# Optimization experiments

Measured on AMD Instinct MI355X. Metric: run time of the kernel, lower is better.

Reference implementation:

```python
import jax, jax.numpy as jnp
import numpy as np

N_NODES = 50000
N_EDGES = 800000
D_IN = 128
D_OUT = 128


def setup_inputs() -> dict:
    key = jax.random.key(0)
    k1, k2, k3, k4, k5 = jax.random.split(key, 5)
    # xavier-uniform-like scale for the two linear layers (gain for relu ~ sqrt(2))
    bound = float(np.sqrt(2.0) * np.sqrt(6.0 / (D_IN + D_OUT)))
    return {
        "feat": jax.random.normal(k1, (N_NODES, D_IN), dtype=jnp.float32),
        "w_neigh": jax.random.uniform(k2, (D_OUT, D_IN), minval=-bound, maxval=bound, dtype=jnp.float32),
        "w_self": jax.random.uniform(k3, (D_OUT, D_IN), minval=-bound, maxval=bound, dtype=jnp.float32),
        "b_self": jnp.zeros((D_OUT,), dtype=jnp.float32),
        "rows": jax.random.randint(k4, (N_EDGES,), 0, N_NODES, dtype=jnp.int32),  # src node per edge
        "cols": jax.random.randint(k5, (N_EDGES,), 0, N_NODES, dtype=jnp.int32),  # dst node per edge
    }


def reference(feat, w_neigh, w_self, b_self, rows, cols):
    n = feat.shape[0]
    # srcdata = fc_neigh(feat): [N, D_OUT]
    srcdata = feat @ w_neigh.T
    # deg[j] = A.sum(0)[j] = in-degree of destination j (column sums)
    deg = jax.ops.segment_sum(jnp.ones_like(cols, dtype=feat.dtype), cols, num_segments=n)
    # dstdata = (A @ diag(deg)^-1).T @ srcdata  ==  mean over incoming src neighbors
    agg = jax.ops.segment_sum(srcdata[rows], cols, num_segments=n)  # [N, D_OUT]
    dstdata = agg / jnp.where(deg > 0, deg, 1.0)[:, None]
    # rst = fc_self(h_self) + dstdata
    return feat @ w_self.T + b_self + dstdata
```

## Files before the change

kernel.cpp:

```cpp
#include <hip/hip_runtime.h>
#include <hip/hip_bf16.h>

#define D 128
#define CAP 64
#define TILE 16

typedef __attribute__((ext_vector_type(8))) short bf16x8;
typedef __attribute__((ext_vector_type(4))) float floatx4;
typedef __attribute__((ext_vector_type(2))) float floatx2;

__device__ __forceinline__ unsigned short f2bf(float f) {
    unsigned int u = __float_as_uint(f);
    return (unsigned short)((u + 0x7fffu + ((u >> 16) & 1u)) >> 16);
}

__global__ __launch_bounds__(256) void zero_kernel(int* __restrict__ p, int n) {
    int i = blockIdx.x * 256 + threadIdx.x;
    if (i < n) p[i] = 0;
}

__global__ __launch_bounds__(256) void prep_fill_kernel(
    const float* __restrict__ feat,
    const float* __restrict__ w_self,
    const float* __restrict__ w_neigh,
    const int* __restrict__ rows,
    const int* __restrict__ cols,
    unsigned int* __restrict__ feat_q,
    unsigned short* __restrict__ ws_h,
    unsigned short* __restrict__ wn_h,
    int* __restrict__ cursor,
    unsigned short* __restrict__ slots,
    int n_nodes, int n_edges)
{
    const int b = blockIdx.x;
    const int tid = threadIdx.x;
    const int role = b % 3;

    if (role < 2) {
        int pb = (b / 3) * 2 + role;
        int i  = pb * 256 + tid;
        if (i < n_nodes * 32) {
            float4 v = *(const float4*)&feat[(long long)4 * i];
            int q = __builtin_amdgcn_cvt_pk_fp8_f32(v.x, v.y, 0, false);
            q = __builtin_amdgcn_cvt_pk_fp8_f32(v.z, v.w, q, true);
            feat_q[i] = (unsigned int)q;
        }
    } else {
        int fb = b / 3;
        int e  = fb * 256 + tid;
        if (e < n_edges) {
            int c = cols[e];
            int p = atomicAdd(&cursor[c], 1);
            if (p < CAP) slots[c * CAP + p] = (unsigned short)rows[e];
        }
        if (fb < 32) {
            int i = fb * 256 + tid;
            int j = i & 4095;
            const float* src = (i < 4096) ? w_self : w_neigh;
            unsigned short* dst = (i < 4096) ? ws_h : wn_h;
            float4 v = *(const float4*)&src[4 * j];
            ushort4 o;
            o.x = f2bf(v.x); o.y = f2bf(v.y); o.z = f2bf(v.z); o.w = f2bf(v.w);
            *(ushort4*)&dst[4 * j] = o;
        }
    }
}

__global__ __launch_bounds__(256, 6) void agg_gemm_kernel(
    const float* __restrict__ feat,
    const unsigned int* __restrict__ feat_q,
    const int* __restrict__ cursor,
    const unsigned short* __restrict__ slots,
    const unsigned short* __restrict__ ws_h,
    const unsigned short* __restrict__ wn_h,
    const float* __restrict__ b_self,
    float* __restrict__ out,
    int n_nodes)
{
    __shared__ unsigned short s_agg[TILE][136];
    __shared__ int s_deg[TILE];

    const int tid  = threadIdx.x;
    const int row0 = blockIdx.x * TILE;

    if (tid < TILE) {
        int node = row0 + tid;
        int d = 0;
        if (node < n_nodes) {
            d = cursor[node];
            if (d > CAP) d = CAP;
        }
        s_deg[tid] = d;
    }
    __syncthreads();

    {
        const int nl  = tid >> 4;
        const int t16 = tid & 15;
        const int sub = t16 & 1;
        const int ln  = t16 >> 1;
        const int deg = s_deg[nl];

        float acc[16];
        #pragma unroll
        for (int i = 0; i < 16; ++i) acc[i] = 0.f;

        const unsigned short* slotp = slots + (long long)(row0 + nl) * CAP;

        for (int k0 = 0; k0 < deg; k0 += 16) {
            uint4 s0 = *(const uint4*)(slotp + k0);
            uint4 s1 = *(const uint4*)(slotp + k0 + 8);
            unsigned int sv[8] = {s0.x, s0.y, s0.z, s0.w, s1.x, s1.y, s1.z, s1.w};
            int cnt = deg - k0; if (cnt > 16) cnt = 16;

            uint4 g[8];
            #pragma unroll
            for (int jj = 0; jj < 8; ++jj) {
                int j = jj * 2 + sub;
                if (j < cnt) {
                    int r = (int)((sv[j >> 1] >> ((j & 1) * 16)) & 0xffffu);
                    g[jj] = *(const uint4*)(feat_q + (long long)r * 32 + ln * 4);
                }
            }
            #pragma unroll
            for (int jj = 0; jj < 8; ++jj) {
                int j = jj * 2 + sub;
                if (j < cnt) {
                    unsigned int wv[4] = {g[jj].x, g[jj].y, g[jj].z, g[jj].w};
                    #pragma unroll
                    for (int c = 0; c < 4; ++c) {
                        floatx2 lo = __builtin_amdgcn_cvt_pk_f32_fp8((int)wv[c], false);
                        floatx2 hi = __builtin_amdgcn_cvt_pk_f32_fp8((int)wv[c], true);
                        acc[c * 4 + 0] += lo.x;
                        acc[c * 4 + 1] += lo.y;
                        acc[c * 4 + 2] += hi.x;
                        acc[c * 4 + 3] += hi.y;
                    }
                }
            }
        }

        #pragma unroll
        for (int i = 0; i < 16; ++i) acc[i] += __shfl_xor(acc[i], 1);

        if (sub == 0) {
            float inv = (deg > 0) ? 1.0f / (float)deg : 0.0f;
            #pragma unroll
            for (int c = 0; c < 4; ++c) {
                ushort4 o;
                o.x = f2bf(acc[c * 4 + 0] * inv);
                o.y = f2bf(acc[c * 4 + 1] * inv);
                o.z = f2bf(acc[c * 4 + 2] * inv);
                o.w = f2bf(acc[c * 4 + 3] * inv);
                *(ushort4*)&s_agg[nl][ln * 16 + c * 4] = o;
            }
        }
    }

    const int wave  = tid >> 6;
    const int lane  = tid & 63;
    const int m     = lane & 15;
    const int quad  = lane >> 4;
    const int kq    = quad * 8;
    const int cbase = wave * 32;

    floatx4 gacc[2];
    gacc[0] = (floatx4){0.f, 0.f, 0.f, 0.f};
    gacc[1] = (floatx4){0.f, 0.f, 0.f, 0.f};

    int rA = row0 + m;
    if (rA > n_nodes - 1) rA = n_nodes - 1;

    #pragma unroll
    for (int kt = 0; kt < 4; ++kt) {
        const int k = kt * 32 + kq;
        float4 f0 = *(const float4*)&feat[(long long)rA * D + k];
        float4 f1 = *(const float4*)&feat[(long long)rA * D + k + 4];
        bf16x8 a;
        a[0] = (short)f2bf(f0.x); a[1] = (short)f2bf(f0.y);
        a[2] = (short)f2bf(f0.z); a[3] = (short)f2bf(f0.w);
        a[4] = (short)f2bf(f1.x); a[5] = (short)f2bf(f1.y);
        a[6] = (short)f2bf(f1.z); a[7] = (short)f2bf(f1.w);
        #pragma unroll
        for (int nt = 0; nt < 2; ++nt) {
            bf16x8 b = *(const bf16x8*)&ws_h[(cbase + nt * 16 + m) * D + k];
            gacc[nt] = __builtin_amdgcn_mfma_f32_16x16x32_bf16(a, b, gacc[nt], 0, 0, 0);
        }
    }

    __syncthreads();

    #pragma unroll
    for (int kt = 0; kt < 4; ++kt) {
        const int k = kt * 32 + kq;
        bf16x8 a = *(const bf16x8*)&s_agg[m][k];
        #pragma unroll
        for (int nt = 0; nt < 2; ++nt) {
            bf16x8 b = *(const bf16x8*)&wn_h[(cbase + nt * 16 + m) * D + k];
            gacc[nt] = __builtin_amdgcn_mfma_f32_16x16x32_bf16(a, b, gacc[nt], 0, 0, 0);
        }
    }

    #pragma unroll
    for (int nt = 0; nt < 2; ++nt) {
        int col = cbase + nt * 16 + m;
        float bias = b_self[col];
        #pragma unroll
        for (int r = 0; r < 4; ++r) {
            int row = row0 + quad * 4 + r;
            if (row < n_nodes)
                out[(long long)row * D + col] = gacc[nt][r] + bias;
        }
    }
}

extern "C" void kernel_launch(void* const* d_in, const int* in_sizes, int n_in,
                              void* d_out, int out_size, void* d_ws, size_t ws_size,
                              hipStream_t stream) {
    const float* feat    = (const float*)d_in[0];
    const float* w_neigh = (const float*)d_in[1];
    const float* w_self  = (const float*)d_in[2];
    const float* b_self  = (const float*)d_in[3];
    const int*   rows    = (const int*)d_in[4];
    const int*   cols    = (const int*)d_in[5];
    float* out = (float*)d_out;

    const int n_nodes = in_sizes[0] / D;
    const int n_edges = in_sizes[4];

    unsigned int*   feat_q = (unsigned int*)d_ws;
    unsigned short* slots  = (unsigned short*)(feat_q + (size_t)n_nodes * 32);
    int* cursor = (int*)(slots + (size_t)n_nodes * CAP);
    unsigned short* ws_h = (unsigned short*)(cursor + n_nodes);
    unsigned short* wn_h = ws_h + 16384;

    zero_kernel<<<(n_nodes + 255) / 256, 256, 0, stream>>>(cursor, n_nodes);

    int nblocks = (n_nodes * 32 + 255) / 256 + (n_edges + 255) / 256;
    prep_fill_kernel<<<nblocks, 256, 0, stream>>>(
        feat, w_self, w_neigh, rows, cols,
        feat_q, ws_h, wn_h, cursor, slots, n_nodes, n_edges);

    agg_gemm_kernel<<<(n_nodes + TILE - 1) / TILE, 256, 0, stream>>>(
        feat, feat_q, cursor, slots, ws_h, wn_h, b_self, out, n_nodes);
}
```

Measured before the change: 180.6 us.

## Precompute bf16 features, branchless padded gather, prefetch slots, relax launch bounds

The prep kernel now also writes a bf16 copy of the features (when workspace allows), so the self-GEMM loads half the bytes and skips per-element conversion. The aggregation loop drops per-neighbor branches by pointing invalid slots at a zeroed padding row, issues all eight gathers unconditionally, and prefetches the next slot chunk while computing. The shared-memory degree stage and its barrier are removed, and launch bounds drop from 6 to 4 waves per SIMD. The cost is an extra 12.8MB bf16 write in prep, plus wasted gathers for nodes whose degree is not a multiple of 16.

```diff
diff --git a/kernel.cpp b/kernel.cpp
--- a/kernel.cpp
+++ b/kernel.cpp
@@ -1,5 +1,4 @@
 #include <hip/hip_runtime.h>
-#include <hip/hip_bf16.h>
 
 #define D 128
 #define CAP 64
@@ -26,6 +25,7 @@
     const int* __restrict__ rows,
     const int* __restrict__ cols,
     unsigned int* __restrict__ feat_q,
+    unsigned short* __restrict__ feat_h,
     unsigned short* __restrict__ ws_h,
     unsigned short* __restrict__ wn_h,
     int* __restrict__ cursor,
@@ -44,6 +44,11 @@
             int q = __builtin_amdgcn_cvt_pk_fp8_f32(v.x, v.y, 0, false);
             q = __builtin_amdgcn_cvt_pk_fp8_f32(v.z, v.w, q, true);
             feat_q[i] = (unsigned int)q;
+            if (feat_h) {
+                ushort4 h;
+                h.x = f2bf(v.x); h.y = f2bf(v.y); h.z = f2bf(v.z); h.w = f2bf(v.w);
+                *(ushort4*)&feat_h[(long long)4 * i] = h;
+            }
         }
     } else {
         int fb = b / 3;
@@ -63,11 +68,15 @@
             o.x = f2bf(v.x); o.y = f2bf(v.y); o.z = f2bf(v.z); o.w = f2bf(v.w);
             *(ushort4*)&dst[4 * j] = o;
         }
-    }
-}
-
-__global__ __launch_bounds__(256, 6) void agg_gemm_kernel(
+        if (fb == 32 && tid < 32)
+            feat_q[(long long)n_nodes * 32 + tid] = 0u;
+    }
+}
+
+template<int USE_FH>
+__global__ __launch_bounds__(256, 4) void agg_gemm_kernel(
     const float* __restrict__ feat,
+    const unsigned short* __restrict__ feat_h,
     const unsigned int* __restrict__ feat_q,
     const int* __restrict__ cursor,
     const unsigned short* __restrict__ slots,
@@ -78,64 +87,65 @@
     int n_nodes)
 {
     __shared__ unsigned short s_agg[TILE][136];
-    __shared__ int s_deg[TILE];
 
     const int tid  = threadIdx.x;
     const int row0 = blockIdx.x * TILE;
-
-    if (tid < TILE) {
-        int node = row0 + tid;
-        int d = 0;
-        if (node < n_nodes) {
-            d = cursor[node];
-            if (d > CAP) d = CAP;
-        }
-        s_deg[tid] = d;
-    }
-    __syncthreads();
 
     {
         const int nl  = tid >> 4;
         const int t16 = tid & 15;
         const int sub = t16 & 1;
         const int ln  = t16 >> 1;
-        const int deg = s_deg[nl];
+        const int node  = row0 + nl;
+        const int snode = (node < n_nodes) ? node : (n_nodes - 1);
+        const unsigned short* slotp = slots + (long long)snode * CAP;
+
+        uint4 s0 = *(const uint4*)(slotp);
+        uint4 s1 = *(const uint4*)(slotp + 8);
+
+        int deg = (node < n_nodes) ? cursor[node] : 0;
+        if (deg > CAP) deg = CAP;
 
         float acc[16];
         #pragma unroll
         for (int i = 0; i < 16; ++i) acc[i] = 0.f;
 
-        const unsigned short* slotp = slots + (long long)(row0 + nl) * CAP;
+        const int sh = sub * 16;
 
         for (int k0 = 0; k0 < deg; k0 += 16) {
-            uint4 s0 = *(const uint4*)(slotp + k0);
-            uint4 s1 = *(const uint4*)(slotp + k0 + 8);
             unsigned int sv[8] = {s0.x, s0.y, s0.z, s0.w, s1.x, s1.y, s1.z, s1.w};
             int cnt = deg - k0; if (cnt > 16) cnt = 16;
 
-            uint4 g[8];
+            int ro[8];
             #pragma unroll
             for (int jj = 0; jj < 8; ++jj) {
                 int j = jj * 2 + sub;
-                if (j < cnt) {
-                    int r = (int)((sv[j >> 1] >> ((j & 1) * 16)) & 0xffffu);
-                    g[jj] = *(const uint4*)(feat_q + (long long)r * 32 + ln * 4);
-                }
-            }
+                int r = (int)((sv[jj] >> sh) & 0xffffu);
+                if (j >= cnt) r = n_nodes;
+                ro[jj] = r * 32 + ln * 4;
+            }
+
+            uint4 g[8];
+            #pragma unroll
+            for (int jj = 0; jj < 8; ++jj)
+                g[jj] = *(const uint4*)(feat_q + ro[jj]);
+
+            if (k0 + 16 < deg) {
+                s0 = *(const uint4*)(slotp + k0 + 16);
+                s1 = *(const uint4*)(slotp + k0 + 24);
+            }
+
             #pragma unroll
             for (int jj = 0; jj < 8; ++jj) {
-                int j = jj * 2 + sub;
-                if (j < cnt) {
-                    unsigned int wv[4] = {g[jj].x, g[jj].y, g[jj].z, g[jj].w};
-                    #pragma unroll
-                    for (int c = 0; c < 4; ++c) {
-                        floatx2 lo = __builtin_amdgcn_cvt_pk_f32_fp8((int)wv[c], false);
-                        floatx2 hi = __builtin_amdgcn_cvt_pk_f32_fp8((int)wv[c], true);
-                        acc[c * 4 + 0] += lo.x;
-                        acc[c * 4 + 1] += lo.y;
-                        acc[c * 4 + 2] += hi.x;
-                        acc[c * 4 + 3] += hi.y;
-                    }
+                unsigned int wv[4] = {g[jj].x, g[jj].y, g[jj].z, g[jj].w};
+                #pragma unroll
+                for (int c = 0; c < 4; ++c) {
+                    floatx2 lo = __builtin_amdgcn_cvt_pk_f32_fp8((int)wv[c], false);
+                    floatx2 hi = __builtin_amdgcn_cvt_pk_f32_fp8((int)wv[c], true);
+                    acc[c * 4 + 0] += lo.x;
+                    acc[c * 4 + 1] += lo.y;
+                    acc[c * 4 + 2] += hi.x;
+                    acc[c * 4 + 3] += hi.y;
                 }
             }
         }
@@ -174,13 +184,17 @@
     #pragma unroll
     for (int kt = 0; kt < 4; ++kt) {
         const int k = kt * 32 + kq;
-        float4 f0 = *(const float4*)&feat[(long long)rA * D + k];
-        float4 f1 = *(const float4*)&feat[(long long)rA * D + k + 4];
         bf16x8 a;
-        a[0] = (short)f2bf(f0.x); a[1] = (short)f2bf(f0.y);
-        a[2] = (short)f2bf(f0.z); a[3] = (short)f2bf(f0.w);
-        a[4] = (short)f2bf(f1.x); a[5] = (short)f2bf(f1.y);
-        a[6] = (short)f2bf(f1.z); a[7] = (short)f2bf(f1.w);
+        if (USE_FH) {
+            a = *(const bf16x8*)&feat_h[(long long)rA * D + k];
+        } else {
+            float4 f0 = *(const float4*)&feat[(long long)rA * D + k];
+            float4 f1 = *(const float4*)&feat[(long long)rA * D + k + 4];
+            a[0] = (short)f2bf(f0.x); a[1] = (short)f2bf(f0.y);
+            a[2] = (short)f2bf(f0.z); a[3] = (short)f2bf(f0.w);
+            a[4] = (short)f2bf(f1.x); a[5] = (short)f2bf(f1.y);
+            a[6] = (short)f2bf(f1.z); a[7] = (short)f2bf(f1.w);
+        }
         #pragma unroll
         for (int nt = 0; nt < 2; ++nt) {
             bf16x8 b = *(const bf16x8*)&ws_h[(cbase + nt * 16 + m) * D + k];
@@ -229,18 +243,25 @@
     const int n_edges = in_sizes[4];
 
     unsigned int*   feat_q = (unsigned int*)d_ws;
-    unsigned short* slots  = (unsigned short*)(feat_q + (size_t)n_nodes * 32);
-    int* cursor = (int*)(slots + (size_t)n_nodes * CAP);
-    unsigned short* ws_h = (unsigned short*)(cursor + n_nodes);
-    unsigned short* wn_h = ws_h + 16384;
+    unsigned short* slots  = (unsigned short*)(feat_q + (size_t)(n_nodes + 1) * 32);
+    int*            cursor = (int*)(slots + (size_t)n_nodes * CAP);
+    unsigned short* ws_h   = (unsigned short*)(cursor + n_nodes);
+    unsigned short* wn_h   = ws_h + 16384;
+    unsigned short* feat_h = wn_h + 16384;
+    size_t needed = (size_t)((char*)(feat_h + (size_t)n_nodes * D) - (char*)d_ws);
+    const bool use_fh = (ws_size >= needed);
 
     zero_kernel<<<(n_nodes + 255) / 256, 256, 0, stream>>>(cursor, n_nodes);
 
     int nblocks = (n_nodes * 32 + 255) / 256 + (n_edges + 255) / 256;
     prep_fill_kernel<<<nblocks, 256, 0, stream>>>(
         feat, w_self, w_neigh, rows, cols,
-        feat_q, ws_h, wn_h, cursor, slots, n_nodes, n_edges);
-
-    agg_gemm_kernel<<<(n_nodes + TILE - 1) / TILE, 256, 0, stream>>>(
-        feat, feat_q, cursor, slots, ws_h, wn_h, b_self, out, n_nodes);
-}
+        feat_q, use_fh ? feat_h : nullptr, ws_h, wn_h, cursor, slots, n_nodes, n_edges);
+
+    if (use_fh)
+        agg_gemm_kernel<1><<<(n_nodes + TILE - 1) / TILE, 256, 0, stream>>>(
+            feat, feat_h, feat_q, cursor, slots, ws_h, wn_h, b_self, out, n_nodes);
+    else
+        agg_gemm_kernel<0><<<(n_nodes + TILE - 1) / TILE, 256, 0, stream>>>(
+            feat, feat_h, feat_q, cursor, slots, ws_h, wn_h, b_self, out, n_nodes);
+}
```

Measured after the change: 207.7 us. +15.0%, slower.
